# Kernel optimization log

Hardware: AMD Instinct MI355X
Metric: run time of the kernel (lower is better)

## Reference

```python
import jax, jax.numpy as jnp
import numpy as np

LEAKY_ALPHA = 0.2      # nn.LeakyReLU(alpha)
NEG_FILL = -9e15       # zero_vec fill value
BN_EPS = 1e-5          # BatchNorm1d default eps

N, F_IN, F_OUT, E = 8192, 256, 64, 262144


def setup_inputs() -> dict:
    key = jax.random.key(0)
    ks = jax.random.split(key, 4)
    h = jax.random.normal(ks[0], (N, F_IN), jnp.float32)
    edge_index = jax.random.randint(ks[1], (2, E), 0, N, dtype=jnp.int64)
    # xavier_uniform-scale params
    W = jax.random.normal(ks[2], (F_IN, F_OUT), jnp.float32) * (1.0 / np.sqrt(F_IN))
    a = jax.random.normal(ks[3], (2 * F_OUT, 1), jnp.float32) * 0.1
    bias = jnp.zeros((F_OUT,), jnp.float32)   # filled with 0.0 in reset_parameters0
    gamma = jnp.ones((F_OUT,), jnp.float32)   # BatchNorm1d weight
    beta = jnp.zeros((F_OUT,), jnp.float32)   # BatchNorm1d bias
    return {"h": h, "edge_index": edge_index, "W": W, "a": a,
            "bias": bias, "gamma": gamma, "beta": beta}


def reference(h, edge_index, W, a, bias, gamma, beta):
    # --- GATLayer (num_heads=1, concat=True, activation=None, dropout off) ---
    hp = h @ W                                   # [N, F_OUT]
    n = hp.shape[0]
    f = hp.shape[1]
    # a_input @ a with a_input[i,j] = [hp_i ; hp_j] decomposes as f1_i + f2_j
    a1, a2 = a[:f, 0], a[f:, 0]
    f1 = hp @ a1                                 # [N]
    f2 = hp @ a2                                 # [N]
    e = jax.nn.leaky_relu(f1[:, None] + f2[None, :], LEAKY_ALPHA)  # [N, N]
    row, col = edge_index[0], edge_index[1]
    adj = jnp.zeros((n, n), dtype=bool).at[row, col].set(True)
    att = jax.nn.softmax(jnp.where(adj, e, NEG_FILL), axis=1)      # [N, N]
    alpha = att[row, col]                        # [E]
    out = att @ hp                               # [N, F_OUT]
    # BatchNorm1d, training mode: batch stats, biased variance
    mean = jnp.mean(out, axis=0)
    var = jnp.mean((out - mean) ** 2, axis=0)
    out = (out - mean) / jnp.sqrt(var + BN_EPS) * gamma + beta
    out = out + bias                             # activation is None
    return out, alpha
```

## Files before the change

### kernel.cpp

```cpp
#include <hip/hip_runtime.h>
#include <stdint.h>

#define N_NODES 8192
#define F_IN    256
#define F_OUT   64
#define N_EDGES 262144
#define LEAKY   0.2f
#define BN_EPSF 1e-5f
#define WPR     256
#define MAXDEG  1024

typedef unsigned int u32;

__device__ __forceinline__ float lrelu(float x) {
    return fmaxf(x, LEAKY * x);
}

__global__ __launch_bounds__(256) void k_hp(
    const float* __restrict__ h, const float* __restrict__ W, const float* __restrict__ a,
    float* __restrict__ hp, float* __restrict__ f1, float* __restrict__ f2)
{
    __shared__ float Wl[F_IN * F_OUT];
    __shared__ float hl[4 * F_IN];
    const int tid = threadIdx.x;
    for (int i = tid; i < F_IN * F_OUT; i += 256) Wl[i] = W[i];

    const int row0 = blockIdx.x * 4;
    const float4* h4 = reinterpret_cast<const float4*>(h + (size_t)row0 * F_IN);
    const float4 hv = h4[tid];
    hl[tid * 4 + 0] = hv.x;
    hl[tid * 4 + 1] = hv.y;
    hl[tid * 4 + 2] = hv.z;
    hl[tid * 4 + 3] = hv.w;
    __syncthreads();

    const int rl = tid >> 6, o = tid & 63;
    const float* hrow = &hl[rl * F_IN];
    float acc = 0.f;
#pragma unroll 8
    for (int k = 0; k < F_IN; ++k)
        acc += hrow[k] * Wl[k * F_OUT + o];

    const int row = row0 + rl;
    hp[row * F_OUT + o] = acc;

    float p1 = acc * a[o];
    float p2 = acc * a[F_OUT + o];
#pragma unroll
    for (int off = 32; off; off >>= 1) {
        p1 += __shfl_xor(p1, off, 64);
        p2 += __shfl_xor(p2, off, 64);
    }
    if (o == 0) { f1[row] = p1; f2[row] = p2; }
}

__global__ __launch_bounds__(256) void k_adj(const int* __restrict__ ei, u32* __restrict__ bm)
{
    const int e = blockIdx.x * 256 + threadIdx.x;
    const int r = ei[e];
    const int c = ei[N_EDGES + e];
    atomicOr(&bm[(size_t)r * WPR + (c >> 5)], 1u << (c & 31));
}

__global__ __launch_bounds__(256) void k_attn(
    const u32* __restrict__ bm, const float* __restrict__ hp,
    const float* __restrict__ f1g, const float* __restrict__ f2g,
    float* __restrict__ Mg, float* __restrict__ Dg, float* __restrict__ outr)
{
    __shared__ int   nbr[4][MAXDEG];
    __shared__ float fv [4][MAXDEG];
    __shared__ int   cnt[4];
    const int tid = threadIdx.x;
    const int w = tid >> 6, lane = tid & 63;
    const int row = blockIdx.x * 4 + w;
    if (lane == 0) cnt[w] = 0;
    __syncthreads();

    float mymax = -1e30f;
    const u32* bmrow = bm + (size_t)row * WPR;
#pragma unroll
    for (int r4 = 0; r4 < 4; ++r4) {
        const int widx = r4 * 64 + lane;
        u32 bits = bmrow[widx];
        if (bits) {
            int pc = __popc(bits);
            int pos = atomicAdd(&cnt[w], pc);
            while (bits) {
                const int b = __ffs(bits) - 1;
                bits &= bits - 1;
                const int j = widx * 32 + b;
                const float v = f2g[j];
                mymax = fmaxf(mymax, v);
                if (pos < MAXDEG) { nbr[w][pos] = j; fv[w][pos] = v; }
                ++pos;
            }
        }
    }
#pragma unroll
    for (int off = 32; off; off >>= 1)
        mymax = fmaxf(mymax, __shfl_xor(mymax, off, 64));
    __syncthreads();

    const int deg = min(cnt[w], MAXDEG);
    const float f1i = f1g[row];
    float M = lrelu(f1i + mymax);
    float den = 0.f, acc = 0.f;
    for (int n = 0; n < deg; ++n) {
        const int j = nbr[w][n];
        const float wgt = __expf(lrelu(f1i + fv[w][n]) - M);
        den += wgt;
        acc += wgt * hp[j * F_OUT + lane];
    }
    if (deg == 0) { den = 1.f; M = 0.f; acc = 0.f; }
    outr[row * F_OUT + lane] = acc / den;
    if (lane == 0) { Mg[row] = M; Dg[row] = den; }
}

__global__ __launch_bounds__(256) void k_bnstats(
    const float* __restrict__ outr, float* __restrict__ meang, float* __restrict__ rstdg)
{
    __shared__ float ss[256], ss2[256];
    const int o = blockIdx.x, tid = threadIdx.x;
    float s = 0.f, s2 = 0.f;
    for (int i = tid; i < N_NODES; i += 256) {
        const float v = outr[i * F_OUT + o];
        s += v; s2 += v * v;
    }
    ss[tid] = s; ss2[tid] = s2;
    __syncthreads();
    for (int st = 128; st; st >>= 1) {
        if (tid < st) { ss[tid] += ss[tid + st]; ss2[tid] += ss2[tid + st]; }
        __syncthreads();
    }
    if (tid == 0) {
        const float mean = ss[0] * (1.f / N_NODES);
        const float var = ss2[0] * (1.f / N_NODES) - mean * mean;
        meang[o] = mean;
        rstdg[o] = rsqrtf(var + BN_EPSF);
    }
}

__global__ __launch_bounds__(256) void k_bnapply(
    const float* __restrict__ outr, const float* __restrict__ meang,
    const float* __restrict__ rstdg, const float* __restrict__ gamma,
    const float* __restrict__ beta, const float* __restrict__ bias,
    float* __restrict__ out)
{
    const int idx = blockIdx.x * 256 + threadIdx.x;
    const int o = idx & 63;
    out[idx] = (outr[idx] - meang[o]) * rstdg[o] * gamma[o] + beta[o] + bias[o];
}

__global__ __launch_bounds__(256) void k_alpha(
    const int* __restrict__ ei, const float* __restrict__ f1g,
    const float* __restrict__ f2g, const float* __restrict__ Mg,
    const float* __restrict__ Dg, float* __restrict__ out)
{
    const int e = blockIdx.x * 256 + threadIdx.x;
    const int r = ei[e];
    const int c = ei[N_EDGES + e];
    out[N_NODES * F_OUT + e] = __expf(lrelu(f1g[r] + f2g[c]) - Mg[r]) / Dg[r];
}

extern "C" void kernel_launch(void* const* d_in, const int* in_sizes, int n_in,
                              void* d_out, int out_size, void* d_ws, size_t ws_size,
                              hipStream_t stream) {
    const float* h     = (const float*)d_in[0];
    const int*   ei    = (const int*)  d_in[1];
    const float* W     = (const float*)d_in[2];
    const float* a     = (const float*)d_in[3];
    const float* bias  = (const float*)d_in[4];
    const float* gamma = (const float*)d_in[5];
    const float* beta  = (const float*)d_in[6];
    float* out = (float*)d_out;

    char* ws = (char*)d_ws;
    float* hp    = (float*)(ws + 0);
    float* f1    = (float*)(ws + 2097152);
    float* f2    = (float*)(ws + 2129920);
    float* Mg    = (float*)(ws + 2162688);
    float* Dg    = (float*)(ws + 2195456);
    float* outr  = (float*)(ws + 2228224);
    float* meang = (float*)(ws + 4325376);
    float* rstdg = (float*)(ws + 4325632);
    u32*   bm    = (u32*)  (ws + 4325888);
    if (ws_size < (size_t)4325888 + (size_t)N_NODES * WPR * 4) return;

    hipMemsetAsync(bm, 0, (size_t)N_NODES * WPR * 4, stream);
    k_hp     <<<N_NODES / 4, 256, 0, stream>>>(h, W, a, hp, f1, f2);
    k_adj    <<<N_EDGES / 256, 256, 0, stream>>>(ei, bm);
    k_attn   <<<N_NODES / 4, 256, 0, stream>>>(bm, hp, f1, f2, Mg, Dg, outr);
    k_bnstats<<<F_OUT, 256, 0, stream>>>(outr, meang, rstdg);
    k_bnapply<<<(N_NODES * F_OUT) / 256, 256, 0, stream>>>(outr, meang, rstdg, gamma, beta, bias, out);
    k_alpha  <<<N_EDGES / 256, 256, 0, stream>>>(ei, f1, f2, Mg, Dg, out);
}
```

Measured before the change: 142.2 us.

## Retile projection GEMM, spread attention row over block, parallelize BN stats

The projection kernel now computes 32 rows per block using a transposed, padded W tile in shared memory and float4 reads, so each W load is reused across 8 rows. The attention kernel assigns one block per row and splits the neighbor loop across four wavefronts, with cross-wave reductions in shared memory, to improve parallelism and occupancy. BN statistics move from 64 single-feature blocks to 256 partial-sum blocks that use float atomics, and the finalization folds into the apply kernel. MAXDEG drops to 256, which is safe for the expected degree of 32 but truncates rows with more neighbors.

```diff
diff --git a/kernel.cpp b/kernel.cpp
--- a/kernel.cpp
+++ b/kernel.cpp
@@ -8,7 +8,8 @@
 #define LEAKY   0.2f
 #define BN_EPSF 1e-5f
 #define WPR     256
-#define MAXDEG  1024
+#define MAXDEG  256
+#define WT_LD   260
 
 typedef unsigned int u32;
 
@@ -20,38 +21,49 @@
     const float* __restrict__ h, const float* __restrict__ W, const float* __restrict__ a,
     float* __restrict__ hp, float* __restrict__ f1, float* __restrict__ f2)
 {
-    __shared__ float Wl[F_IN * F_OUT];
-    __shared__ float hl[4 * F_IN];
+    __shared__ float Wt[F_OUT * WT_LD];
+    __shared__ float hl[32 * F_IN];
     const int tid = threadIdx.x;
-    for (int i = tid; i < F_IN * F_OUT; i += 256) Wl[i] = W[i];
-
-    const int row0 = blockIdx.x * 4;
+
+#pragma unroll
+    for (int i = tid; i < F_IN * F_OUT; i += 256)
+        Wt[(i & 63) * WT_LD + (i >> 6)] = W[i];
+
+    const int row0 = blockIdx.x * 32;
+    float4* hl4 = reinterpret_cast<float4*>(hl);
     const float4* h4 = reinterpret_cast<const float4*>(h + (size_t)row0 * F_IN);
-    const float4 hv = h4[tid];
-    hl[tid * 4 + 0] = hv.x;
-    hl[tid * 4 + 1] = hv.y;
-    hl[tid * 4 + 2] = hv.z;
-    hl[tid * 4 + 3] = hv.w;
-    __syncthreads();
-
-    const int rl = tid >> 6, o = tid & 63;
-    const float* hrow = &hl[rl * F_IN];
-    float acc = 0.f;
-#pragma unroll 8
-    for (int k = 0; k < F_IN; ++k)
-        acc += hrow[k] * Wl[k * F_OUT + o];
-
-    const int row = row0 + rl;
-    hp[row * F_OUT + o] = acc;
-
-    float p1 = acc * a[o];
-    float p2 = acc * a[F_OUT + o];
-#pragma unroll
-    for (int off = 32; off; off >>= 1) {
-        p1 += __shfl_xor(p1, off, 64);
-        p2 += __shfl_xor(p2, off, 64);
-    }
-    if (o == 0) { f1[row] = p1; f2[row] = p2; }
+#pragma unroll
+    for (int p = 0; p < 8; ++p)
+        hl4[tid + p * 256] = h4[tid + p * 256];
+    __syncthreads();
+
+    const int w = tid >> 6, o = tid & 63;
+    const int rbase = w * 8;
+    float acc[8] = {0.f, 0.f, 0.f, 0.f, 0.f, 0.f, 0.f, 0.f};
+
+    for (int q = 0; q < 64; ++q) {
+        const float4 wv = *reinterpret_cast<const float4*>(&Wt[o * WT_LD + 4 * q]);
+#pragma unroll
+        for (int r = 0; r < 8; ++r) {
+            const float4 hv = *reinterpret_cast<const float4*>(&hl[(rbase + r) * F_IN + 4 * q]);
+            acc[r] += wv.x * hv.x + wv.y * hv.y + wv.z * hv.z + wv.w * hv.w;
+        }
+    }
+
+    const float a1 = a[o], a2 = a[F_OUT + o];
+#pragma unroll
+    for (int r = 0; r < 8; ++r) {
+        const int row = row0 + rbase + r;
+        hp[row * F_OUT + o] = acc[r];
+        float p1 = acc[r] * a1;
+        float p2 = acc[r] * a2;
+#pragma unroll
+        for (int off = 32; off; off >>= 1) {
+            p1 += __shfl_xor(p1, off, 64);
+            p2 += __shfl_xor(p2, off, 64);
+        }
+        if (o == 0) { f1[row] = p1; f2[row] = p2; }
+    }
 }
 
 __global__ __launch_bounds__(256) void k_adj(const int* __restrict__ ei, u32* __restrict__ bm)
@@ -67,88 +79,110 @@
     const float* __restrict__ f1g, const float* __restrict__ f2g,
     float* __restrict__ Mg, float* __restrict__ Dg, float* __restrict__ outr)
 {
-    __shared__ int   nbr[4][MAXDEG];
-    __shared__ float fv [4][MAXDEG];
-    __shared__ int   cnt[4];
+    __shared__ int   nbr[MAXDEG];
+    __shared__ float fv [MAXDEG];
+    __shared__ int   cnt;
+    __shared__ float redm[4];
+    __shared__ float accs[4][F_OUT];
+    __shared__ float dens[4];
     const int tid = threadIdx.x;
     const int w = tid >> 6, lane = tid & 63;
-    const int row = blockIdx.x * 4 + w;
-    if (lane == 0) cnt[w] = 0;
-    __syncthreads();
-
+    const int row = blockIdx.x;
+    if (tid == 0) cnt = 0;
+    __syncthreads();
+
+    u32 bits = bm[(size_t)row * WPR + tid];
     float mymax = -1e30f;
-    const u32* bmrow = bm + (size_t)row * WPR;
-#pragma unroll
-    for (int r4 = 0; r4 < 4; ++r4) {
-        const int widx = r4 * 64 + lane;
-        u32 bits = bmrow[widx];
-        if (bits) {
-            int pc = __popc(bits);
-            int pos = atomicAdd(&cnt[w], pc);
-            while (bits) {
-                const int b = __ffs(bits) - 1;
-                bits &= bits - 1;
-                const int j = widx * 32 + b;
-                const float v = f2g[j];
-                mymax = fmaxf(mymax, v);
-                if (pos < MAXDEG) { nbr[w][pos] = j; fv[w][pos] = v; }
-                ++pos;
-            }
+    if (bits) {
+        int pos = atomicAdd(&cnt, __popc(bits));
+        while (bits) {
+            const int b = __ffs(bits) - 1;
+            bits &= bits - 1;
+            const int j = tid * 32 + b;
+            const float v = f2g[j];
+            mymax = fmaxf(mymax, v);
+            if (pos < MAXDEG) { nbr[pos] = j; fv[pos] = v; }
+            ++pos;
         }
     }
 #pragma unroll
     for (int off = 32; off; off >>= 1)
         mymax = fmaxf(mymax, __shfl_xor(mymax, off, 64));
-    __syncthreads();
-
-    const int deg = min(cnt[w], MAXDEG);
+    if (lane == 0) redm[w] = mymax;
+    __syncthreads();
+
+    const int deg = min(cnt, MAXDEG);
     const float f1i = f1g[row];
-    float M = lrelu(f1i + mymax);
+    const float M = lrelu(f1i + fmaxf(fmaxf(redm[0], redm[1]), fmaxf(redm[2], redm[3])));
+
     float den = 0.f, acc = 0.f;
-    for (int n = 0; n < deg; ++n) {
-        const int j = nbr[w][n];
-        const float wgt = __expf(lrelu(f1i + fv[w][n]) - M);
+    for (int n = w; n < deg; n += 4) {
+        const int j = nbr[n];
+        const float wgt = __expf(lrelu(f1i + fv[n]) - M);
         den += wgt;
         acc += wgt * hp[j * F_OUT + lane];
     }
-    if (deg == 0) { den = 1.f; M = 0.f; acc = 0.f; }
-    outr[row * F_OUT + lane] = acc / den;
-    if (lane == 0) { Mg[row] = M; Dg[row] = den; }
-}
-
-__global__ __launch_bounds__(256) void k_bnstats(
-    const float* __restrict__ outr, float* __restrict__ meang, float* __restrict__ rstdg)
-{
-    __shared__ float ss[256], ss2[256];
-    const int o = blockIdx.x, tid = threadIdx.x;
-    float s = 0.f, s2 = 0.f;
-    for (int i = tid; i < N_NODES; i += 256) {
-        const float v = outr[i * F_OUT + o];
-        s += v; s2 += v * v;
-    }
-    ss[tid] = s; ss2[tid] = s2;
-    __syncthreads();
-    for (int st = 128; st; st >>= 1) {
-        if (tid < st) { ss[tid] += ss[tid + st]; ss2[tid] += ss2[tid + st]; }
+    accs[w][lane] = acc;
+    if (lane == 0) dens[w] = den;
+    __syncthreads();
+
+    if (w == 0) {
+        float av = accs[0][lane] + accs[1][lane] + accs[2][lane] + accs[3][lane];
+        float d = dens[0] + dens[1] + dens[2] + dens[3];
+        float Mw = M;
+        if (deg == 0) { d = 1.f; Mw = 0.f; av = 0.f; }
+        outr[row * F_OUT + lane] = av / d;
+        if (lane == 0) { Mg[row] = Mw; Dg[row] = d; }
+    }
+}
+
+__global__ __launch_bounds__(256) void k_bnpart(
+    const float* __restrict__ outr, float* __restrict__ Sacc, float* __restrict__ Qacc)
+{
+    __shared__ float4 sp[16][16], sq[16][16];
+    const int tid = threadIdx.x;
+    const int m = tid >> 4, f4 = tid & 15;
+    const float4* o4 = reinterpret_cast<const float4*>(outr);
+    float4 s = {0.f, 0.f, 0.f, 0.f}, q = {0.f, 0.f, 0.f, 0.f};
+#pragma unroll
+    for (int p = 0; p < 2; ++p) {
+        const float4 v = o4[blockIdx.x * 512 + tid + p * 256];
+        s.x += v.x; s.y += v.y; s.z += v.z; s.w += v.w;
+        q.x += v.x * v.x; q.y += v.y * v.y; q.z += v.z * v.z; q.w += v.w * v.w;
+    }
+    sp[m][f4] = s; sq[m][f4] = q;
+    for (int st = 8; st; st >>= 1) {
         __syncthreads();
-    }
-    if (tid == 0) {
-        const float mean = ss[0] * (1.f / N_NODES);
-        const float var = ss2[0] * (1.f / N_NODES) - mean * mean;
-        meang[o] = mean;
-        rstdg[o] = rsqrtf(var + BN_EPSF);
+        if (m < st) {
+            float4 xs = sp[m + st][f4], xq = sq[m + st][f4];
+            float4 cs = sp[m][f4], cq = sq[m][f4];
+            cs.x += xs.x; cs.y += xs.y; cs.z += xs.z; cs.w += xs.w;
+            cq.x += xq.x; cq.y += xq.y; cq.z += xq.z; cq.w += xq.w;
+            sp[m][f4] = cs; sq[m][f4] = cq;
+        }
+    }
+    __syncthreads();
+    if (tid < 16) {
+        const float4 cs = sp[0][tid], cq = sq[0][tid];
+        atomicAdd(&Sacc[tid * 4 + 0], cs.x); atomicAdd(&Sacc[tid * 4 + 1], cs.y);
+        atomicAdd(&Sacc[tid * 4 + 2], cs.z); atomicAdd(&Sacc[tid * 4 + 3], cs.w);
+        atomicAdd(&Qacc[tid * 4 + 0], cq.x); atomicAdd(&Qacc[tid * 4 + 1], cq.y);
+        atomicAdd(&Qacc[tid * 4 + 2], cq.z); atomicAdd(&Qacc[tid * 4 + 3], cq.w);
     }
 }
 
 __global__ __launch_bounds__(256) void k_bnapply(
-    const float* __restrict__ outr, const float* __restrict__ meang,
-    const float* __restrict__ rstdg, const float* __restrict__ gamma,
+    const float* __restrict__ outr, const float* __restrict__ Sacc,
+    const float* __restrict__ Qacc, const float* __restrict__ gamma,
     const float* __restrict__ beta, const float* __restrict__ bias,
     float* __restrict__ out)
 {
     const int idx = blockIdx.x * 256 + threadIdx.x;
     const int o = idx & 63;
-    out[idx] = (outr[idx] - meang[o]) * rstdg[o] * gamma[o] + beta[o] + bias[o];
+    const float mean = Sacc[o] * (1.f / N_NODES);
+    const float var = Qacc[o] * (1.f / N_NODES) - mean * mean;
+    const float rstd = rsqrtf(var + BN_EPSF);
+    out[idx] = (outr[idx] - mean) * rstd * gamma[o] + beta[o] + bias[o];
 }
 
 __global__ __launch_bounds__(256) void k_alpha(
@@ -181,16 +215,16 @@
     float* Mg    = (float*)(ws + 2162688);
     float* Dg    = (float*)(ws + 2195456);
     float* outr  = (float*)(ws + 2228224);
-    float* meang = (float*)(ws + 4325376);
-    float* rstdg = (float*)(ws + 4325632);
+    float* Sacc  = (float*)(ws + 4325376);
+    float* Qacc  = (float*)(ws + 4325632);
     u32*   bm    = (u32*)  (ws + 4325888);
     if (ws_size < (size_t)4325888 + (size_t)N_NODES * WPR * 4) return;
 
-    hipMemsetAsync(bm, 0, (size_t)N_NODES * WPR * 4, stream);
-    k_hp     <<<N_NODES / 4, 256, 0, stream>>>(h, W, a, hp, f1, f2);
+    hipMemsetAsync(ws + 4325376, 0, 512 + (size_t)N_NODES * WPR * 4, stream);
+    k_hp     <<<N_NODES / 32, 256, 0, stream>>>(h, W, a, hp, f1, f2);
     k_adj    <<<N_EDGES / 256, 256, 0, stream>>>(ei, bm);
-    k_attn   <<<N_NODES / 4, 256, 0, stream>>>(bm, hp, f1, f2, Mg, Dg, outr);
-    k_bnstats<<<F_OUT, 256, 0, stream>>>(outr, meang, rstdg);
-    k_bnapply<<<(N_NODES * F_OUT) / 256, 256, 0, stream>>>(outr, meang, rstdg, gamma, beta, bias, out);
+    k_attn   <<<N_NODES, 256, 0, stream>>>(bm, hp, f1, f2, Mg, Dg, outr);
+    k_bnpart <<<N_NODES / 32, 256, 0, stream>>>(outr, Sacc, Qacc);
+    k_bnapply<<<(N_NODES * F_OUT) / 256, 256, 0, stream>>>(outr, Sacc, Qacc, gamma, beta, bias, out);
     k_alpha  <<<N_EDGES / 256, 256, 0, stream>>>(ei, f1, f2, Mg, Dg, out);
 }
```

Measured after the change: 155.4 us. +9.2%, slower.
